# Kernel tuning notes

Hardware: AMD Instinct MI355X
Metric: run time of the kernel (lower is better)

Reference implementation:

```python
import jax, jax.numpy as jnp
import numpy as np

R = 16
LORA_ALPHA = 32
SCALING = LORA_ALPHA / R  # use_rslora=False -> alpha/r = 2.0


def fwht(x):
    """Normalized fast Walsh-Hadamard transform along last axis (power-of-2 dim)."""
    n = x.shape[-1]
    batch = x.shape[:-1]
    h = 1
    while h < n:  # static loop, log2(n) iterations
        x = x.reshape(*batch, n // (2 * h), 2, h)
        a = x[..., 0, :]
        b = x[..., 1, :]
        x = jnp.stack([a + b, a - b], axis=-2).reshape(*batch, n)
        h *= 2
    return x * np.float32(1.0 / np.sqrt(n))


def quant_int8_ste(x):
    """Simulated symmetric per-row int8 quantization with straight-through estimator."""
    s = jnp.max(jnp.abs(x), axis=-1, keepdims=True) * np.float32(1.0 / 127.0)
    s = jnp.maximum(s, np.float32(1e-8))
    q = jnp.clip(jnp.round(x / s), -127.0, 127.0) * s
    return x + jax.lax.stop_gradient(q - x)


def setup_inputs() -> dict:
    key = jax.random.key(0)
    k1, k2, k3, k4 = jax.random.split(key, 4)
    B, S, D_in, D_out = 4, 2048, 4096, 4096
    x = jax.random.normal(k1, (B, S, D_in), dtype=jnp.float32)
    weight = jax.random.normal(k2, (D_out, D_in), dtype=jnp.float32) * np.float32(0.02)
    lora_A = jax.random.normal(k3, (R, D_in), dtype=jnp.float32) * np.float32(0.02)
    lora_B = jax.random.normal(k4, (D_out, R), dtype=jnp.float32) * np.float32(0.02)
    return {"x": x, "weight": weight, "lora_A": lora_A, "lora_B": lora_B}


def reference(x, weight, lora_A, lora_B):
    B, S, D_in = x.shape
    x2 = x.reshape(-1, D_in)  # [B*S, D_in]
    # Hadamard-rotate + quantize both operands (rotation is orthogonal, so
    # (xH)(WH)^T == xW^T up to quantization error) then GEMM.
    xq = quant_int8_ste(fwht(x2))          # [B*S, D_in]
    wq = quant_int8_ste(fwht(weight))      # [D_out, D_in]
    out = xq @ wq.T                        # [B*S, D_out]
    # LoRA side path (dropout p=0): B(A x) * scaling
    lora = (x2 @ lora_A.T) @ lora_B.T * np.float32(SCALING)
    return (out + lora).reshape(B, S, -1)
```

## Files before the change

### kernel.cpp

```cpp
#include <hip/hip_runtime.h>
#include <stdint.h>

typedef int v4i __attribute__((ext_vector_type(4)));

#define DSR(d, b, O) \
  asm volatile("ds_read_b128 %0, %1 offset:" O : "=v"(d) : "v"(b))
#define DSW(b, O, v) \
  asm volatile("ds_write_b128 %0, %1 offset:" O ::"v"(b), "v"(v) : "memory")
#define LGKM0()                                        \
  do {                                                 \
    asm volatile("s_waitcnt lgkmcnt(0)" ::: "memory"); \
    __builtin_amdgcn_sched_barrier(0);                 \
  } while (0)

__device__ __forceinline__ void fwht16(float v[16]) {
#pragma unroll
  for (int h = 1; h < 16; h <<= 1) {
#pragma unroll
    for (int i = 0; i < 16; ++i) {
      if (!(i & h)) {
        float a = v[i], b = v[i | h];
        v[i] = a + b;
        v[i | h] = a - b;
      }
    }
  }
}

__device__ __forceinline__ void fwht_row_load(const float* __restrict__ xr, int t,
                                              float v[16]) {
  const float4* p = reinterpret_cast<const float4*>(xr) + t * 4;
  float4 a = p[0], b = p[1], c = p[2], d = p[3];
  v[0] = a.x; v[1] = a.y; v[2] = a.z; v[3] = a.w;
  v[4] = b.x; v[5] = b.y; v[6] = b.z; v[7] = b.w;
  v[8] = c.x; v[9] = c.y; v[10] = c.z; v[11] = c.w;
  v[12] = d.x; v[13] = d.y; v[14] = d.z; v[15] = d.w;
}

__device__ __forceinline__ void fwht4096(float v[16], float* lds, int t) {
  fwht16(v);
#pragma unroll
  for (int e = 0; e < 16; ++e) {
    int idx = t * 16 + e;
    lds[idx + (idx >> 5)] = v[e];
  }
  __syncthreads();
#pragma unroll
  for (int e = 0; e < 16; ++e) {
    int idx = ((t >> 4) << 8) + (e << 4) + (t & 15);
    v[e] = lds[idx + (idx >> 5)];
  }
  fwht16(v);
#pragma unroll
  for (int e = 0; e < 16; ++e) {
    int idx = ((t >> 4) << 8) + (e << 4) + (t & 15);
    lds[idx + (idx >> 5)] = v[e];
  }
  __syncthreads();
#pragma unroll
  for (int e = 0; e < 16; ++e) {
    int idx = (e << 8) + t;
    v[e] = lds[idx + (idx >> 5)];
  }
  fwht16(v);
#pragma unroll
  for (int e = 0; e < 16; ++e) v[e] *= 0.015625f;
}

__global__ __launch_bounds__(256) void fwht_quant_kernel(const float* __restrict__ X,
                                                         int8_t* __restrict__ Q,
                                                         float* __restrict__ S) {
  const int row = blockIdx.x;
  const int t = threadIdx.x;
  __shared__ __align__(16) float lds[4224];
  __shared__ float wred[4];

  float v[16];
  fwht_row_load(X + (size_t)row * 4096, t, v);
  fwht4096(v, lds, t);

  float m = 0.f;
#pragma unroll
  for (int e = 0; e < 16; ++e) m = fmaxf(m, fabsf(v[e]));
#pragma unroll
  for (int off = 32; off > 0; off >>= 1) m = fmaxf(m, __shfl_xor(m, off));
  if ((t & 63) == 0) wred[t >> 6] = m;
  __syncthreads();
  m = fmaxf(fmaxf(wred[0], wred[1]), fmaxf(wred[2], wred[3]));
  const float s = fmaxf(m * (1.0f / 127.0f), 1e-8f);
  if (t == 0) S[row] = s;

  __syncthreads();
  char* b8 = (char*)lds;
#pragma unroll
  for (int e = 0; e < 16; ++e) {
    float q = rintf(v[e] / s);
    q = fminf(fmaxf(q, -127.f), 127.f);
    int idx = (e << 8) + t;
    b8[idx + ((idx >> 8) << 4)] = (char)(int)q;
  }
  __syncthreads();
  int4 pack = *reinterpret_cast<const int4*>(b8 + t * 16 + ((t >> 4) << 4));
  reinterpret_cast<int4*>(Q + (size_t)row * 4096)[t] = pack;
}

__global__ __launch_bounds__(256) void lora_mfma_kernel(const int8_t* __restrict__ Qx,
                                                        const int8_t* __restrict__ Qa,
                                                        int* __restrict__ tqp) {
  const int lane = threadIdx.x & 63;
  const int wv = threadIdx.x >> 6;
  const int m0 = (blockIdx.x * 4 + wv) * 16;
  const int kc = blockIdx.y;
  const int8_t* ax =
      Qx + (size_t)(m0 + (lane & 15)) * 4096 + kc * 512 + ((lane >> 4) << 4);
  const int8_t* bx = Qa + (size_t)(lane & 15) * 4096 + kc * 512 + ((lane >> 4) << 4);
  v4i acc = {0, 0, 0, 0};
#pragma unroll
  for (int s = 0; s < 8; ++s) {
    v4i a = *reinterpret_cast<const v4i*>(ax + s * 64);
    v4i b = *reinterpret_cast<const v4i*>(bx + s * 64);
    acc = __builtin_amdgcn_mfma_i32_16x16x64_i8(a, b, acc, 0, 0, 0);
  }
  int* tp = tqp + ((size_t)kc * 8192 + m0) * 16;
#pragma unroll
  for (int rr = 0; rr < 4; ++rr)
    tp[((lane >> 4) * 4 + rr) * 16 + (lane & 15)] = acc[rr];
}

__global__ __launch_bounds__(256) void lora_t_reduce_kernel(const int* __restrict__ tqp,
                                                            const float* __restrict__ Sx,
                                                            const float* __restrict__ Sa,
                                                            float* __restrict__ tmat) {
  int i = blockIdx.x * 256 + threadIdx.x;
  int row = i >> 4, r = i & 15;
  int s = 0;
#pragma unroll
  for (int kc = 0; kc < 8; ++kc) s += tqp[(size_t)kc * 131072 + i];
  tmat[i] = (float)s * Sx[row] * Sa[r];
}

__global__ __launch_bounds__(1024, 4) void gemm_i8_kernel(
    const int8_t* __restrict__ Aq, const int8_t* __restrict__ Bq,
    const float* __restrict__ Sx, const float* __restrict__ Sw,
    const float* __restrict__ Tm, const float* __restrict__ LB,
    float* __restrict__ out) {
  __shared__ __align__(16) char smem[65536];

  const int tid = threadIdx.x;
  const int lane = tid & 63;
  const int w = tid >> 6;
  const int wm = w >> 2;
  const int wn = w & 3;

  int bid = (int)blockIdx.x;
  bid = (bid & 7) * 64 + (bid >> 3);
  const int bm = bid >> 4;
  const int bn = bid & 15;

  const int sr = tid >> 2;
  const int sc = tid & 3;
  const uint32_t sbase = (uint32_t)(uintptr_t)(void*)smem;
  const uint32_t wAddr =
      sbase + (uint32_t)(sr * 64 + ((sc ^ ((sr >> 1) & 3)) << 4));
  const int8_t* Agp = Aq + (size_t)bm * 256 * 4096 + (size_t)sr * 4096 + sc * 16;
  const int8_t* Bgp = Bq + (size_t)bn * 256 * 4096 + (size_t)sr * 4096 + sc * 16;

  const int cc = lane >> 4;
  const int ar0 = wm * 64 + (lane & 15);
  const int br0 = wn * 64 + (lane & 15);
  const uint32_t aBase = sbase + (uint32_t)(ar0 * 64 + ((cc ^ ((ar0 >> 1) & 3)) << 4));
  const uint32_t bBase = sbase + (uint32_t)(br0 * 64 + ((cc ^ ((br0 >> 1) & 3)) << 4));

  v4i acc[4][4];
#pragma unroll
  for (int i = 0; i < 4; ++i)
#pragma unroll
    for (int n = 0; n < 4; ++n) {
      v4i z = {0, 0, 0, 0};
      acc[i][n] = z;
    }

#define MFMA16()                                                                     \
  do {                                                                               \
    __builtin_amdgcn_s_setprio(1);                                                   \
    _Pragma("unroll") for (int i = 0; i < 4; ++i) _Pragma("unroll") for (int n = 0;  \
                                                                        n < 4; ++n)  \
        acc[i][n] = __builtin_amdgcn_mfma_i32_16x16x64_i8(af[i], bf[n], acc[i][n],   \
                                                          0, 0, 0);                  \
    __builtin_amdgcn_s_setprio(0);                                                   \
  } while (0)

  v4i eA = *reinterpret_cast<const v4i*>(Agp);
  v4i eB = *reinterpret_cast<const v4i*>(Bgp);
  v4i oA = *reinterpret_cast<const v4i*>(Agp + 64);
  v4i oB = *reinterpret_cast<const v4i*>(Bgp + 64);
  DSW(wAddr, "0", eA);
  DSW(wAddr, "16384", eB);
  LGKM0();
  __builtin_amdgcn_s_barrier();
  __builtin_amdgcn_sched_barrier(0);

#pragma unroll 1
  for (int i = 0; i < 32; ++i) {
    v4i af[4], bf[4];
    if (i < 31) {
      const int kb = (2 * i + 2) << 6;
      eA = *reinterpret_cast<const v4i*>(Agp + kb);
      eB = *reinterpret_cast<const v4i*>(Bgp + kb);
    }
    __builtin_amdgcn_sched_barrier(0);
    DSR(af[0], aBase, "0");
    DSR(af[1], aBase, "1024");
    DSR(af[2], aBase, "2048");
    DSR(af[3], aBase, "3072");
    DSR(bf[0], bBase, "16384");
    DSR(bf[1], bBase, "17408");
    DSR(bf[2], bBase, "18432");
    DSR(bf[3], bBase, "19456");
    LGKM0();
    MFMA16();
    DSW(wAddr, "32768", oA);
    DSW(wAddr, "49152", oB);
    LGKM0();
    __builtin_amdgcn_s_barrier();
    __builtin_amdgcn_sched_barrier(0);

    if (i < 31) {
      const int kb = (2 * i + 3) << 6;
      oA = *reinterpret_cast<const v4i*>(Agp + kb);
      oB = *reinterpret_cast<const v4i*>(Bgp + kb);
    }
    __builtin_amdgcn_sched_barrier(0);
    DSR(af[0], aBase, "32768");
    DSR(af[1], aBase, "33792");
    DSR(af[2], aBase, "34816");
    DSR(af[3], aBase, "35840");
    DSR(bf[0], bBase, "49152");
    DSR(bf[1], bBase, "50176");
    DSR(bf[2], bBase, "51200");
    DSR(bf[3], bBase, "52224");
    LGKM0();
    MFMA16();
    if (i < 31) {
      DSW(wAddr, "0", eA);
      DSW(wAddr, "16384", eB);
      LGKM0();
      __builtin_amdgcn_s_barrier();
      __builtin_amdgcn_sched_barrier(0);
    }
  }

  __syncthreads();
  float* tl = (float*)smem;
  float* bl = (float*)(smem + 17408);
  {
    int r = tid >> 2, q4 = (tid & 3) * 4;
    float4 tv = *reinterpret_cast<const float4*>(Tm + (size_t)(bm * 256 + r) * 16 + q4);
    tl[r * 17 + q4 + 0] = tv.x;
    tl[r * 17 + q4 + 1] = tv.y;
    tl[r * 17 + q4 + 2] = tv.z;
    tl[r * 17 + q4 + 3] = tv.w;
    float4 bv = *reinterpret_cast<const float4*>(LB + (size_t)(bn * 256 + r) * 16 + q4);
    bl[r * 17 + q4 + 0] = bv.x;
    bl[r * 17 + q4 + 1] = bv.y;
    bl[r * 17 + q4 + 2] = bv.z;
    bl[r * 17 + q4 + 3] = bv.w;
  }
  __syncthreads();

  float blv[4][16], swv[4];
#pragma unroll
  for (int ni = 0; ni < 4; ++ni) {
    int cl = wn * 64 + ni * 16 + (lane & 15);
    swv[ni] = Sw[bn * 256 + cl];
#pragma unroll
    for (int q = 0; q < 16; ++q) blv[ni][q] = bl[cl * 17 + q];
  }
#pragma unroll
  for (int mi = 0; mi < 4; ++mi) {
#pragma unroll
    for (int rr = 0; rr < 4; ++rr) {
      int rl = wm * 64 + mi * 16 + (lane >> 4) * 4 + rr;
      float sxv = Sx[bm * 256 + rl];
      float tv[16];
#pragma unroll
      for (int q = 0; q < 16; ++q) tv[q] = tl[rl * 17 + q];
      float* orow = out + (size_t)(bm * 256 + rl) * 4096 + bn * 256;
#pragma unroll
      for (int ni = 0; ni < 4; ++ni) {
        float dot = 0.f;
#pragma unroll
        for (int q = 0; q < 16; ++q) dot = fmaf(tv[q], blv[ni][q], dot);
        int cl = wn * 64 + ni * 16 + (lane & 15);
        orow[cl] = sxv * swv[ni] * (float)acc[mi][ni][rr] + 2.0f * dot;
      }
    }
  }
}

extern "C" void kernel_launch(void* const* d_in, const int* in_sizes, int n_in,
                              void* d_out, int out_size, void* d_ws, size_t ws_size,
                              hipStream_t stream) {
  const float* x = (const float*)d_in[0];
  const float* wgt = (const float*)d_in[1];
  const float* lA = (const float*)d_in[2];
  const float* lB = (const float*)d_in[3];
  float* out = (float*)d_out;

  char* ws = (char*)d_ws;
  int8_t* qx = (int8_t*)ws;
  int8_t* qw = (int8_t*)(ws + 33554432);
  float* sx = (float*)(ws + 50331648);
  float* sw = (float*)(ws + 50364416);
  float* tmat = (float*)(ws + 50380800);
  int* tqp = (int*)(ws + 50905088);
  int8_t* qa = (int8_t*)(ws + 55099392);
  float* sa = (float*)(ws + 55164928);

  fwht_quant_kernel<<<8192, 256, 0, stream>>>(x, qx, sx);
  fwht_quant_kernel<<<4096, 256, 0, stream>>>(wgt, qw, sw);
  fwht_quant_kernel<<<16, 256, 0, stream>>>(lA, qa, sa);
  lora_mfma_kernel<<<dim3(128, 8), 256, 0, stream>>>(qx, qa, tqp);
  lora_t_reduce_kernel<<<512, 256, 0, stream>>>(tqp, sx, sa, tmat);
  gemm_i8_kernel<<<512, 1024, 0, stream>>>(qx, qw, sx, sw, tmat, lB, out);
}
```

Baseline: 315.6 us.

## Rework int8 GEMM with direct global-to-LDS loads and triple-buffered pipeline

The int8 GEMM moves from 1024-thread blocks with 256x256 tiles to 512-thread blocks with 256x128 tiles. Operand staging now uses global_load_lds to copy straight into shared memory, with a swizzled source offset and a three-stage ring buffer. B fragments for the next step are prefetched during the current MFMAs. The quantize kernel also stops packing bytes through LDS and writes int8 values straight to global, trading coalesced 16-byte stores for byte stores and two fewer barriers. The risks are more A-tile reloads from global memory and the correctness of the manual vmcnt/lgkmcnt waits.

```diff
diff --git a/kernel.cpp b/kernel.cpp
--- a/kernel.cpp
+++ b/kernel.cpp
@@ -3,15 +3,15 @@
 
 typedef int v4i __attribute__((ext_vector_type(4)));
 
-#define DSR(d, b, O) \
-  asm volatile("ds_read_b128 %0, %1 offset:" O : "=v"(d) : "v"(b))
-#define DSW(b, O, v) \
-  asm volatile("ds_write_b128 %0, %1 offset:" O ::"v"(b), "v"(v) : "memory")
-#define LGKM0()                                        \
-  do {                                                 \
-    asm volatile("s_waitcnt lgkmcnt(0)" ::: "memory"); \
-    __builtin_amdgcn_sched_barrier(0);                 \
-  } while (0)
+#define GLD_LDS16(gp, lp)                                                              \
+  __builtin_amdgcn_global_load_lds((const __attribute__((address_space(1))) void*)(gp), \
+                                   (__attribute__((address_space(3))) void*)(lp), 16, 0, 0)
+
+__device__ __forceinline__ v4i lds_read_b128(uint32_t off) {
+  v4i r;
+  asm volatile("ds_read_b128 %0, %1" : "=v"(r) : "v"(off));
+  return r;
+}
 
 __device__ __forceinline__ void fwht16(float v[16]) {
 #pragma unroll
@@ -72,7 +72,7 @@
                                                          float* __restrict__ S) {
   const int row = blockIdx.x;
   const int t = threadIdx.x;
-  __shared__ __align__(16) float lds[4224];
+  __shared__ float lds[4224];
   __shared__ float wred[4];
 
   float v[16];
@@ -89,19 +89,13 @@
   m = fmaxf(fmaxf(wred[0], wred[1]), fmaxf(wred[2], wred[3]));
   const float s = fmaxf(m * (1.0f / 127.0f), 1e-8f);
   if (t == 0) S[row] = s;
-
-  __syncthreads();
-  char* b8 = (char*)lds;
+  int8_t* qr = Q + (size_t)row * 4096;
 #pragma unroll
   for (int e = 0; e < 16; ++e) {
     float q = rintf(v[e] / s);
     q = fminf(fmaxf(q, -127.f), 127.f);
-    int idx = (e << 8) + t;
-    b8[idx + ((idx >> 8) << 4)] = (char)(int)q;
-  }
-  __syncthreads();
-  int4 pack = *reinterpret_cast<const int4*>(b8 + t * 16 + ((t >> 4) << 4));
-  reinterpret_cast<int4*>(Q + (size_t)row * 4096)[t] = pack;
+    qr[(e << 8) + t] = (int8_t)(int)q;
+  }
 }
 
 __global__ __launch_bounds__(256) void lora_mfma_kernel(const int8_t* __restrict__ Qx,
@@ -139,37 +133,54 @@
   tmat[i] = (float)s * Sx[row] * Sa[r];
 }
 
-__global__ __launch_bounds__(1024, 4) void gemm_i8_kernel(
+__global__ __launch_bounds__(512, 4) void gemm_i8_kernel(
     const int8_t* __restrict__ Aq, const int8_t* __restrict__ Bq,
     const float* __restrict__ Sx, const float* __restrict__ Sw,
     const float* __restrict__ Tm, const float* __restrict__ LB,
     float* __restrict__ out) {
-  __shared__ __align__(16) char smem[65536];
+  __shared__ __align__(16) char smem[73728];
 
   const int tid = threadIdx.x;
   const int lane = tid & 63;
   const int w = tid >> 6;
-  const int wm = w >> 2;
-  const int wn = w & 3;
+  const int wm = w >> 1;
+  const int wn = w & 1;
 
   int bid = (int)blockIdx.x;
-  bid = (bid & 7) * 64 + (bid >> 3);
-  const int bm = bid >> 4;
-  const int bn = bid & 15;
-
-  const int sr = tid >> 2;
-  const int sc = tid & 3;
+  bid = (bid & 7) * 128 + (bid >> 3);
+  const int bm = bid >> 5;
+  const int bn = bid & 31;
+
+  const int8_t* Ag = Aq + (size_t)bm * 256 * 4096;
+  const int8_t* Bg = Bq + (size_t)bn * 128 * 4096;
+
   const uint32_t sbase = (uint32_t)(uintptr_t)(void*)smem;
-  const uint32_t wAddr =
-      sbase + (uint32_t)(sr * 64 + ((sc ^ ((sr >> 1) & 3)) << 4));
-  const int8_t* Agp = Aq + (size_t)bm * 256 * 4096 + (size_t)sr * 4096 + sc * 16;
-  const int8_t* Bgp = Bq + (size_t)bn * 256 * 4096 + (size_t)sr * 4096 + sc * 16;
-
+
+  const uint32_t srcOff = (uint32_t)(((lane & 3) ^ ((lane >> 3) & 3)) << 4);
+  const uint32_t gA0 = (uint32_t)((w * 32 + (lane >> 2)) * 4096) + srcOff;
+  const uint32_t gA1 = gA0 + 16 * 4096;
+  const uint32_t gB0 = (uint32_t)((w * 16 + (lane >> 2)) * 4096) + srcOff;
+
+#define STAGE_STEP(s, bufbase)                                           \
+  do {                                                                   \
+    const uint32_t kb = (uint32_t)(s) << 6;                              \
+    GLD_LDS16(Ag + kb + gA0, smem + (bufbase) + w * 2048);               \
+    GLD_LDS16(Ag + kb + gA1, smem + (bufbase) + w * 2048 + 1024);        \
+    GLD_LDS16(Bg + kb + gB0, smem + (bufbase) + 16384 + w * 1024);       \
+  } while (0)
+
+  int aoff[4], boff[4];
   const int cc = lane >> 4;
-  const int ar0 = wm * 64 + (lane & 15);
-  const int br0 = wn * 64 + (lane & 15);
-  const uint32_t aBase = sbase + (uint32_t)(ar0 * 64 + ((cc ^ ((ar0 >> 1) & 3)) << 4));
-  const uint32_t bBase = sbase + (uint32_t)(br0 * 64 + ((cc ^ ((br0 >> 1) & 3)) << 4));
+#pragma unroll
+  for (int mi = 0; mi < 4; ++mi) {
+    int r = wm * 64 + mi * 16 + (lane & 15);
+    aoff[mi] = r * 64 + ((cc ^ ((r >> 1) & 3)) << 4);
+  }
+#pragma unroll
+  for (int ni = 0; ni < 4; ++ni) {
+    int r = wn * 64 + ni * 16 + (lane & 15);
+    boff[ni] = 16384 + r * 64 + ((cc ^ ((r >> 1) & 3)) << 4);
+  }
 
   v4i acc[4][4];
 #pragma unroll
@@ -180,87 +191,87 @@
       acc[i][n] = z;
     }
 
-#define MFMA16()                                                                     \
-  do {                                                                               \
-    __builtin_amdgcn_s_setprio(1);                                                   \
-    _Pragma("unroll") for (int i = 0; i < 4; ++i) _Pragma("unroll") for (int n = 0;  \
-                                                                        n < 4; ++n)  \
-        acc[i][n] = __builtin_amdgcn_mfma_i32_16x16x64_i8(af[i], bf[n], acc[i][n],   \
-                                                          0, 0, 0);                  \
-    __builtin_amdgcn_s_setprio(0);                                                   \
+#define MFMA8(M0)                                                              \
+  do {                                                                         \
+    __builtin_amdgcn_s_setprio(1);                                             \
+    _Pragma("unroll") for (int ii = 0; ii < 2; ++ii)                           \
+        _Pragma("unroll") for (int n = 0; n < 4; ++n)                          \
+        acc[(M0) + ii][n] = __builtin_amdgcn_mfma_i32_16x16x64_i8(             \
+            af[(M0) + ii], bf[n], acc[(M0) + ii][n], 0, 0, 0);                 \
+    __builtin_amdgcn_s_setprio(0);                                             \
   } while (0)
 
-  v4i eA = *reinterpret_cast<const v4i*>(Agp);
-  v4i eB = *reinterpret_cast<const v4i*>(Bgp);
-  v4i oA = *reinterpret_cast<const v4i*>(Agp + 64);
-  v4i oB = *reinterpret_cast<const v4i*>(Bgp + 64);
-  DSW(wAddr, "0", eA);
-  DSW(wAddr, "16384", eB);
-  LGKM0();
+  STAGE_STEP(0, 0);
+  STAGE_STEP(1, 24576);
+  asm volatile("s_waitcnt vmcnt(3)" ::: "memory");
   __builtin_amdgcn_s_barrier();
   __builtin_amdgcn_sched_barrier(0);
 
+  v4i bf[4], bfp[4];
+#pragma unroll
+  for (int n = 0; n < 4; ++n) bf[n] = lds_read_b128(sbase + boff[n]);
+
+  uint32_t bc = 0, bn1 = 24576, bn2 = 49152;
+
 #pragma unroll 1
-  for (int i = 0; i < 32; ++i) {
-    v4i af[4], bf[4];
-    if (i < 31) {
-      const int kb = (2 * i + 2) << 6;
-      eA = *reinterpret_cast<const v4i*>(Agp + kb);
-      eB = *reinterpret_cast<const v4i*>(Bgp + kb);
-    }
+  for (int t = 0; t < 64; ++t) {
+    if (t <= 61) STAGE_STEP(t + 2, bn2);
+
+    const uint32_t R = sbase + bc;
+    v4i af[4];
+    af[0] = lds_read_b128(R + aoff[0]);
+    af[1] = lds_read_b128(R + aoff[1]);
+    af[2] = lds_read_b128(R + aoff[2]);
+    af[3] = lds_read_b128(R + aoff[3]);
+    asm volatile("s_waitcnt lgkmcnt(2)" ::: "memory");
     __builtin_amdgcn_sched_barrier(0);
-    DSR(af[0], aBase, "0");
-    DSR(af[1], aBase, "1024");
-    DSR(af[2], aBase, "2048");
-    DSR(af[3], aBase, "3072");
-    DSR(bf[0], bBase, "16384");
-    DSR(bf[1], bBase, "17408");
-    DSR(bf[2], bBase, "18432");
-    DSR(bf[3], bBase, "19456");
-    LGKM0();
-    MFMA16();
-    DSW(wAddr, "32768", oA);
-    DSW(wAddr, "49152", oB);
-    LGKM0();
+    MFMA8(0);
+    asm volatile("s_waitcnt lgkmcnt(0)" ::: "memory");
+    __builtin_amdgcn_sched_barrier(0);
+
+    if (t <= 61)
+      asm volatile("s_waitcnt vmcnt(3)" ::: "memory");
+    else if (t == 62)
+      asm volatile("s_waitcnt vmcnt(0)" ::: "memory");
     __builtin_amdgcn_s_barrier();
     __builtin_amdgcn_sched_barrier(0);
 
-    if (i < 31) {
-      const int kb = (2 * i + 3) << 6;
-      oA = *reinterpret_cast<const v4i*>(Agp + kb);
-      oB = *reinterpret_cast<const v4i*>(Bgp + kb);
-    }
-    __builtin_amdgcn_sched_barrier(0);
-    DSR(af[0], aBase, "32768");
-    DSR(af[1], aBase, "33792");
-    DSR(af[2], aBase, "34816");
-    DSR(af[3], aBase, "35840");
-    DSR(bf[0], bBase, "49152");
-    DSR(bf[1], bBase, "50176");
-    DSR(bf[2], bBase, "51200");
-    DSR(bf[3], bBase, "52224");
-    LGKM0();
-    MFMA16();
-    if (i < 31) {
-      DSW(wAddr, "0", eA);
-      DSW(wAddr, "16384", eB);
-      LGKM0();
-      __builtin_amdgcn_s_barrier();
+    if (t < 63) {
+      const uint32_t Rn = sbase + bn1;
+      bfp[0] = lds_read_b128(Rn + boff[0]);
+      bfp[1] = lds_read_b128(Rn + boff[1]);
+      bfp[2] = lds_read_b128(Rn + boff[2]);
+      bfp[3] = lds_read_b128(Rn + boff[3]);
+    }
+
+    MFMA8(2);
+    if (t < 63) {
+      asm volatile("s_waitcnt lgkmcnt(0)" ::: "memory");
       __builtin_amdgcn_sched_barrier(0);
-    }
+#pragma unroll
+      for (int n = 0; n < 4; ++n) bf[n] = bfp[n];
+    }
+
+    uint32_t tmp = bc;
+    bc = bn1;
+    bn1 = bn2;
+    bn2 = tmp;
   }
 
   __syncthreads();
   float* tl = (float*)smem;
   float* bl = (float*)(smem + 17408);
-  {
-    int r = tid >> 2, q4 = (tid & 3) * 4;
+  for (int i = tid; i < 1024; i += 512) {
+    int r = i >> 2, q4 = (i & 3) * 4;
     float4 tv = *reinterpret_cast<const float4*>(Tm + (size_t)(bm * 256 + r) * 16 + q4);
     tl[r * 17 + q4 + 0] = tv.x;
     tl[r * 17 + q4 + 1] = tv.y;
     tl[r * 17 + q4 + 2] = tv.z;
     tl[r * 17 + q4 + 3] = tv.w;
-    float4 bv = *reinterpret_cast<const float4*>(LB + (size_t)(bn * 256 + r) * 16 + q4);
+  }
+  if (tid < 512) {
+    int r = tid >> 2, q4 = (tid & 3) * 4;
+    float4 bv = *reinterpret_cast<const float4*>(LB + (size_t)(bn * 128 + r) * 16 + q4);
     bl[r * 17 + q4 + 0] = bv.x;
     bl[r * 17 + q4 + 1] = bv.y;
     bl[r * 17 + q4 + 2] = bv.z;
@@ -272,7 +283,7 @@
 #pragma unroll
   for (int ni = 0; ni < 4; ++ni) {
     int cl = wn * 64 + ni * 16 + (lane & 15);
-    swv[ni] = Sw[bn * 256 + cl];
+    swv[ni] = Sw[bn * 128 + cl];
 #pragma unroll
     for (int q = 0; q < 16; ++q) blv[ni][q] = bl[cl * 17 + q];
   }
@@ -285,7 +296,7 @@
       float tv[16];
 #pragma unroll
       for (int q = 0; q < 16; ++q) tv[q] = tl[rl * 17 + q];
-      float* orow = out + (size_t)(bm * 256 + rl) * 4096 + bn * 256;
+      float* orow = out + (size_t)(bm * 256 + rl) * 4096 + bn * 128;
 #pragma unroll
       for (int ni = 0; ni < 4; ++ni) {
         float dot = 0.f;
@@ -322,5 +333,5 @@
   fwht_quant_kernel<<<16, 256, 0, stream>>>(lA, qa, sa);
   lora_mfma_kernel<<<dim3(128, 8), 256, 0, stream>>>(qx, qa, tqp);
   lora_t_reduce_kernel<<<512, 256, 0, stream>>>(tqp, sx, sa, tmat);
-  gemm_i8_kernel<<<512, 1024, 0, stream>>>(qx, qw, sx, sw, tmat, lB, out);
-}
+  gemm_i8_kernel<<<1024, 512, 0, stream>>>(qx, qw, sx, sw, tmat, lB, out);
+}
```

After: 304.4 us. -3.5%, faster.
